# Kernel optimization log

Hardware: AMD Instinct MI355X
Metric: run time of the kernel (lower is better)

The kernel has to match this reference:

```python
import jax, jax.numpy as jnp
import numpy as np

N_NODES = 50000
N_EDGES = 800000
IN_C, HID_C, OUT_C = 128, 128, 64


def setup_inputs() -> dict:
    key = jax.random.key(0)
    ks = jax.random.split(key, 8)
    sc_in = 1.0 / np.sqrt(IN_C)
    sc_hid = 1.0 / np.sqrt(HID_C)
    return {
        "x": jax.random.normal(ks[0], (N_NODES, IN_C), dtype=jnp.float32),
        "edge_index": jax.random.randint(ks[1], (2, N_EDGES), 0, N_NODES, dtype=jnp.int64),
        "W1_l": jax.random.normal(ks[2], (IN_C, HID_C), dtype=jnp.float32) * sc_in,
        "b1": jnp.zeros((HID_C,), dtype=jnp.float32),
        "W1_r": jax.random.normal(ks[3], (IN_C, HID_C), dtype=jnp.float32) * sc_in,
        "W2_l": jax.random.normal(ks[4], (HID_C, OUT_C), dtype=jnp.float32) * sc_hid,
        "b2": jnp.zeros((OUT_C,), dtype=jnp.float32),
        "W2_r": jax.random.normal(ks[5], (HID_C, OUT_C), dtype=jnp.float32) * sc_hid,
    }


def _sage_conv(x, src, dst, W_l, b, W_r, num_nodes):
    # gather neighbor features along edges: messages flow src -> dst
    msg = x[src]                                             # [E, C]
    agg = jax.ops.segment_sum(msg, dst, num_segments=num_nodes)
    cnt = jax.ops.segment_sum(jnp.ones((src.shape[0],), x.dtype), dst,
                              num_segments=num_nodes)
    mean = agg / jnp.maximum(cnt, 1.0)[:, None]              # mean aggregation
    # PyG SAGEConv: lin_l(aggregated) + lin_r(root); bias on lin_l only
    return mean @ W_l + b + x @ W_r


def reference(x, edge_index, W1_l, b1, W1_r, W2_l, b2, W2_r):
    src, dst = edge_index[0], edge_index[1]
    n = x.shape[0]
    h = jax.nn.relu(_sage_conv(x, src, dst, W1_l, b1, W1_r, n))
    # dropout(p=0.2) is identity at inference (training=False)
    return _sage_conv(h, src, dst, W2_l, b2, W2_r, n)
```

## Files before the change

kernel.cpp:

```cpp
#include <hip/hip_runtime.h>

#define N_NODES 50000
#define N_EDGES 800000
#define IN_C 128
#define HID_C 128
#define OUT_C 64

#define NBUCK 500
#define NODES_PER_BUCK 100
#define BCAP 2560
#define BA_CHUNK 8192
#define BA_BLOCKS ((N_EDGES + BA_CHUNK - 1) / BA_CHUNK)

typedef __bf16 bf16x8 __attribute__((ext_vector_type(8)));
typedef __bf16 bf16x4 __attribute__((ext_vector_type(4)));
typedef float  f32x4  __attribute__((ext_vector_type(4)));


__global__ __launch_bounds__(256) void init_cursor_kernel(int* cursor) {
    int i = blockIdx.x * 256 + threadIdx.x;
    if (i < NBUCK) cursor[i] = i * BCAP;
}

__global__ __launch_bounds__(256) void bucketA_kernel(const int* __restrict__ src,
                                                      const int* __restrict__ dst,
                                                      int* __restrict__ cursor,
                                                      uint2* __restrict__ ebuf) {
    __shared__ int cnt[NBUCK];
    __shared__ int gbase[NBUCK];
    __shared__ int lcur[NBUCK];
    const int t = threadIdx.x;
    for (int i = t; i < NBUCK; i += 256) cnt[i] = 0;
    __syncthreads();
    const int e0 = blockIdx.x * BA_CHUNK;
    const int e1 = (e0 + BA_CHUNK < N_EDGES) ? e0 + BA_CHUNK : N_EDGES;
    for (int e = e0 + t; e < e1; e += 256)
        atomicAdd(&cnt[dst[e] / NODES_PER_BUCK], 1);
    __syncthreads();
    for (int i = t; i < NBUCK; i += 256) {
        gbase[i] = atomicAdd(&cursor[i], cnt[i]);
        lcur[i] = 0;
    }
    __syncthreads();
    for (int e = e0 + t; e < e1; e += 256) {
        int d = dst[e];
        int b = d / NODES_PER_BUCK;
        int idx = gbase[b] + atomicAdd(&lcur[b], 1);
        if (idx < (b + 1) * BCAP)
            ebuf[idx] = make_uint2((unsigned)src[e], (unsigned)d);
    }
}

__global__ __launch_bounds__(512) void scan500_kernel(const int* __restrict__ cursor,
                                                      int* __restrict__ bbase,
                                                      int* __restrict__ bsize) {
    __shared__ int sh[512];
    const int t = threadIdx.x;
    int v = 0;
    if (t < NBUCK) {
        v = cursor[t] - t * BCAP;
        if (v > BCAP) v = BCAP;
    }
    sh[t] = v;
    __syncthreads();
    for (int off = 1; off < 512; off <<= 1) {
        int u = (t >= off) ? sh[t - off] : 0;
        __syncthreads();
        sh[t] += u;
        __syncthreads();
    }
    if (t < NBUCK) { bbase[t] = sh[t] - v; bsize[t] = v; }
}

__global__ __launch_bounds__(256) void bucketB_kernel(const uint2* __restrict__ ebuf,
                                                      const int* __restrict__ bbase,
                                                      const int* __restrict__ bsize,
                                                      int* __restrict__ row_ptr,
                                                      int* __restrict__ srcs) {
    __shared__ int deg[NODES_PER_BUCK];
    __shared__ int ofs[NODES_PER_BUCK + 1];
    const int b = blockIdx.x, t = threadIdx.x;
    const int node0 = b * NODES_PER_BUCK;
    const int m = bsize[b];
    const int rbase = bbase[b];
    const uint2* eb = ebuf + (size_t)b * BCAP;
    for (int i = t; i < NODES_PER_BUCK; i += 256) deg[i] = 0;
    __syncthreads();
    for (int i = t; i < m; i += 256)
        atomicAdd(&deg[(int)eb[i].y - node0], 1);
    __syncthreads();
    if (t == 0) {
        int s = 0;
        for (int i = 0; i < NODES_PER_BUCK; ++i) { ofs[i] = s; s += deg[i]; }
        ofs[NODES_PER_BUCK] = s;
    }
    __syncthreads();
    for (int i = t; i < NODES_PER_BUCK; i += 256) row_ptr[node0 + i] = rbase + ofs[i];
    if (b == 0 && t == 0) row_ptr[N_NODES] = N_EDGES;
    for (int i = t; i < NODES_PER_BUCK; i += 256) deg[i] = ofs[i];
    __syncthreads();
    for (int i = t; i < m; i += 256) {
        uint2 p = eb[i];
        int d = (int)p.y - node0;
        int pos = atomicAdd(&deg[d], 1);
        srcs[rbase + pos] = (int)p.x;
    }
}


__global__ __launch_bounds__(256) void f32_to_bf16_kernel(const float* __restrict__ in,
                                                          __bf16* __restrict__ out, int n4) {
    int i = blockIdx.x * 256 + threadIdx.x;
    if (i >= n4) return;
    float4 v = ((const float4*)in)[i];
    bf16x4 o = { (__bf16)v.x, (__bf16)v.y, (__bf16)v.z, (__bf16)v.w };
    ((bf16x4*)out)[i] = o;
}

__global__ __launch_bounds__(256) void pack_w_kernel(const float* __restrict__ W1l,
                                                     const float* __restrict__ W1r,
                                                     const float* __restrict__ W2l,
                                                     const float* __restrict__ W2r,
                                                     __bf16* __restrict__ W1T,
                                                     __bf16* __restrict__ W2T) {
    int i = blockIdx.x * 256 + threadIdx.x;
    if (i < 128 * 256) {
        int n = i >> 8, kk = i & 255;
        float v = (kk < 128) ? W1l[kk * 128 + n] : W1r[(kk - 128) * 128 + n];
        W1T[i] = (__bf16)v;
    } else {
        int j = i - 128 * 256;
        if (j < 128 * 128) {
            int n = j >> 7, k = j & 127;
            float v = (n < 64) ? W2l[k * 64 + n] : W2r[k * 64 + (n - 64)];
            W2T[j] = (__bf16)v;
        }
    }
}

__global__ __launch_bounds__(256) void agg_x_kernel(const __bf16* __restrict__ xb,
                                                    const int* __restrict__ row_ptr,
                                                    const int* __restrict__ srcs,
                                                    __bf16* __restrict__ m1) {
    const int wid = threadIdx.x >> 6, lane = threadIdx.x & 63;
    const int n = blockIdx.x * 4 + wid;
    if (n >= N_NODES) return;
    const int beg = row_ptr[n], end = row_ptr[n + 1];
    const int grp = lane >> 4;
    const int c   = lane & 15;
    float acc[8] = {};
    for (int s = beg + grp; s < end; s += 4) {
        int u = srcs[s];
        bf16x8 v = *(const bf16x8*)(xb + (size_t)u * 128 + c * 8);
#pragma unroll
        for (int j = 0; j < 8; j++) acc[j] += (float)v[j];
    }
#pragma unroll
    for (int j = 0; j < 8; j++) {
        acc[j] += __shfl_xor(acc[j], 16, 64);
        acc[j] += __shfl_xor(acc[j], 32, 64);
    }
    float cnt = (float)(end - beg);
    if (cnt < 1.f) cnt = 1.f;
    if (grp == 0) {
        bf16x8 o;
#pragma unroll
        for (int j = 0; j < 8; j++) o[j] = (__bf16)(acc[j] / cnt);
        *(bf16x8*)(m1 + (size_t)n * 128 + c * 8) = o;
    }
}

#define LDK 72

__global__ __launch_bounds__(256) void gemm1_kernel(const __bf16* __restrict__ A0,
                                                    const __bf16* __restrict__ A1,
                                                    const __bf16* __restrict__ Bt,
                                                    const float* __restrict__ b1,
                                                    __bf16* __restrict__ h, int M) {
    __shared__ __bf16 As[128 * LDK];
    __shared__ __bf16 Bs[128 * LDK];
    const int tid = threadIdx.x;
    const int row0 = blockIdx.y * 128;
    const int wave = tid >> 6, lane = tid & 63;
    const int wm = (wave & 1) * 64, wn = (wave >> 1) * 64;
    const int lr = lane & 15, quad = lane >> 4;

    f32x4 acc[4][4] = {};

    for (int ks = 0; ks < 256; ks += 64) {
        const __bf16* Asrc = (ks < 128) ? A0 : A1;
        const int kofs = (ks < 128) ? ks : ks - 128;
        for (int i = tid; i < 128 * 8; i += 256) {
            int r = i >> 3, ch = i & 7;
            int gr = row0 + r;
            float4 v = {0.f, 0.f, 0.f, 0.f};
            if (gr < M) v = *(const float4*)(Asrc + (size_t)gr * 128 + kofs + ch * 8);
            *(float4*)(As + r * LDK + ch * 8) = v;
        }
        for (int i = tid; i < 128 * 8; i += 256) {
            int r = i >> 3, ch = i & 7;
            float4 v = *(const float4*)(Bt + (size_t)r * 256 + ks + ch * 8);
            *(float4*)(Bs + r * LDK + ch * 8) = v;
        }
        __syncthreads();
#pragma unroll
        for (int k0 = 0; k0 < 64; k0 += 32) {
            bf16x8 af[4], bfr[4];
#pragma unroll
            for (int mt = 0; mt < 4; mt++)
                af[mt] = *(const bf16x8*)(As + (wm + mt * 16 + lr) * LDK + k0 + quad * 8);
#pragma unroll
            for (int nt = 0; nt < 4; nt++)
                bfr[nt] = *(const bf16x8*)(Bs + (wn + nt * 16 + lr) * LDK + k0 + quad * 8);
#pragma unroll
            for (int mt = 0; mt < 4; mt++)
#pragma unroll
                for (int nt = 0; nt < 4; nt++)
                    acc[mt][nt] = __builtin_amdgcn_mfma_f32_16x16x32_bf16(af[mt], bfr[nt], acc[mt][nt], 0, 0, 0);
        }
        __syncthreads();
    }

#pragma unroll
    for (int mt = 0; mt < 4; mt++) {
#pragma unroll
        for (int r = 0; r < 4; r++) {
            int gr = row0 + wm + mt * 16 + quad * 4 + r;
            if (gr >= M) continue;
#pragma unroll
            for (int nt = 0; nt < 4; nt++) {
                int gc = wn + nt * 16 + lr;
                float v = acc[mt][nt][r] + b1[gc];
                v = v > 0.f ? v : 0.f;
                h[(size_t)gr * 128 + gc] = (__bf16)v;
            }
        }
    }
}

__global__ __launch_bounds__(256) void gemm2_kernel(const __bf16* __restrict__ A,
                                                    const __bf16* __restrict__ Bt,
                                                    __bf16* __restrict__ Y,
                                                    float* __restrict__ Z, int M) {
    __shared__ __bf16 As[128 * LDK];
    __shared__ __bf16 Bs[128 * LDK];
    const int tid = threadIdx.x;
    const int row0 = blockIdx.y * 128;
    const int wave = tid >> 6, lane = tid & 63;
    const int wm = (wave & 1) * 64, wn = (wave >> 1) * 64;
    const int lr = lane & 15, quad = lane >> 4;

    f32x4 acc[4][4] = {};

    for (int ks = 0; ks < 128; ks += 64) {
        for (int i = tid; i < 128 * 8; i += 256) {
            int r = i >> 3, ch = i & 7;
            int gr = row0 + r;
            float4 v = {0.f, 0.f, 0.f, 0.f};
            if (gr < M) v = *(const float4*)(A + (size_t)gr * 128 + ks + ch * 8);
            *(float4*)(As + r * LDK + ch * 8) = v;
        }
        for (int i = tid; i < 128 * 8; i += 256) {
            int r = i >> 3, ch = i & 7;
            float4 v = *(const float4*)(Bt + (size_t)r * 128 + ks + ch * 8);
            *(float4*)(Bs + r * LDK + ch * 8) = v;
        }
        __syncthreads();
#pragma unroll
        for (int k0 = 0; k0 < 64; k0 += 32) {
            bf16x8 af[4], bfr[4];
#pragma unroll
            for (int mt = 0; mt < 4; mt++)
                af[mt] = *(const bf16x8*)(As + (wm + mt * 16 + lr) * LDK + k0 + quad * 8);
#pragma unroll
            for (int nt = 0; nt < 4; nt++)
                bfr[nt] = *(const bf16x8*)(Bs + (wn + nt * 16 + lr) * LDK + k0 + quad * 8);
#pragma unroll
            for (int mt = 0; mt < 4; mt++)
#pragma unroll
                for (int nt = 0; nt < 4; nt++)
                    acc[mt][nt] = __builtin_amdgcn_mfma_f32_16x16x32_bf16(af[mt], bfr[nt], acc[mt][nt], 0, 0, 0);
        }
        __syncthreads();
    }

#pragma unroll
    for (int mt = 0; mt < 4; mt++) {
#pragma unroll
        for (int r = 0; r < 4; r++) {
            int gr = row0 + wm + mt * 16 + quad * 4 + r;
            if (gr >= M) continue;
#pragma unroll
            for (int nt = 0; nt < 4; nt++) {
                int gc = wn + nt * 16 + lr;
                float v = acc[mt][nt][r];
                if (gc < 64) Y[(size_t)gr * 64 + gc] = (__bf16)v;
                else         Z[(size_t)gr * 64 + (gc - 64)] = v;
            }
        }
    }
}

__global__ __launch_bounds__(256) void agg2_kernel(const __bf16* __restrict__ Y,
                                                   const float* __restrict__ Z,
                                                   const int* __restrict__ row_ptr,
                                                   const int* __restrict__ srcs,
                                                   const float* __restrict__ b2,
                                                   float* __restrict__ out) {
    const int wid = threadIdx.x >> 6, lane = threadIdx.x & 63;
    const int n = blockIdx.x * 4 + wid;
    if (n >= N_NODES) return;
    const int beg = row_ptr[n], end = row_ptr[n + 1];
    const int grp = lane >> 3;
    const int c   = lane & 7;
    float acc[8] = {};
    for (int s = beg + grp; s < end; s += 8) {
        int u = srcs[s];
        bf16x8 v = *(const bf16x8*)(Y + (size_t)u * 64 + c * 8);
#pragma unroll
        for (int j = 0; j < 8; j++) acc[j] += (float)v[j];
    }
#pragma unroll
    for (int j = 0; j < 8; j++) {
        acc[j] += __shfl_xor(acc[j], 8, 64);
        acc[j] += __shfl_xor(acc[j], 16, 64);
        acc[j] += __shfl_xor(acc[j], 32, 64);
    }
    float cnt = (float)(end - beg);
    if (cnt < 1.f) cnt = 1.f;
    if (grp == 0) {
#pragma unroll
        for (int j = 0; j < 8; j++) {
            int ch = c * 8 + j;
            out[(size_t)n * 64 + ch] = acc[j] / cnt + b2[ch] + Z[(size_t)n * 64 + ch];
        }
    }
}


extern "C" void kernel_launch(void* const* d_in, const int* in_sizes, int n_in,
                              void* d_out, int out_size, void* d_ws, size_t ws_size,
                              hipStream_t stream) {
    const float* x   = (const float*)d_in[0];
    const int*   ei  = (const int*)d_in[1];
    const float* W1l = (const float*)d_in[2];
    const float* b1  = (const float*)d_in[3];
    const float* W1r = (const float*)d_in[4];
    const float* W2l = (const float*)d_in[5];
    const float* b2  = (const float*)d_in[6];
    const float* W2r = (const float*)d_in[7];
    float* out = (float*)d_out;

    size_t need = 0;
    auto count = [&](size_t bytes) { need += (bytes + 255) & ~(size_t)255; };
    count((size_t)NBUCK * BCAP * 8);
    count((size_t)NBUCK * 4);
    count((size_t)NBUCK * 4);
    count((size_t)NBUCK * 4);
    count((size_t)(N_NODES + 1) * 4);
    count((size_t)N_EDGES * 4);
    count((size_t)N_NODES * 128 * 2);
    count((size_t)128 * 256 * 2);
    count((size_t)128 * 128 * 2);
    count((size_t)N_NODES * 128 * 2);
    count((size_t)N_NODES * 128 * 2);
    count((size_t)N_NODES * 64 * 2);
    count((size_t)N_NODES * 64 * 4);
    if (ws_size < need) return;

    char* ws = (char*)d_ws;
    size_t off = 0;
    auto alloc = [&](size_t bytes) -> void* {
        void* p = ws + off;
        off += (bytes + 255) & ~(size_t)255;
        return p;
    };
    uint2*  ebuf    = (uint2*)alloc((size_t)NBUCK * BCAP * 8);
    int*    cursor  = (int*)alloc((size_t)NBUCK * 4);
    int*    bbase   = (int*)alloc((size_t)NBUCK * 4);
    int*    bsize   = (int*)alloc((size_t)NBUCK * 4);
    int*    row_ptr = (int*)alloc((size_t)(N_NODES + 1) * 4);
    int*    srcs    = (int*)alloc((size_t)N_EDGES * 4);
    __bf16* xb      = (__bf16*)alloc((size_t)N_NODES * 128 * 2);
    __bf16* W1T     = (__bf16*)alloc((size_t)128 * 256 * 2);
    __bf16* W2T     = (__bf16*)alloc((size_t)128 * 128 * 2);
    __bf16* m1      = (__bf16*)alloc((size_t)N_NODES * 128 * 2);
    __bf16* h       = (__bf16*)alloc((size_t)N_NODES * 128 * 2);
    __bf16* Y       = (__bf16*)alloc((size_t)N_NODES * 64 * 2);
    float*  Z       = (float*)alloc((size_t)N_NODES * 64 * 4);

    const int* src = ei;
    const int* dst = ei + N_EDGES;

    init_cursor_kernel<<<(NBUCK + 255) / 256, 256, 0, stream>>>(cursor);
    bucketA_kernel<<<BA_BLOCKS, 256, 0, stream>>>(src, dst, cursor, ebuf);
    scan500_kernel<<<1, 512, 0, stream>>>(cursor, bbase, bsize);
    bucketB_kernel<<<NBUCK, 256, 0, stream>>>(ebuf, bbase, bsize, row_ptr, srcs);

    f32_to_bf16_kernel<<<(N_NODES * 128 / 4 + 255) / 256, 256, 0, stream>>>(x, xb, N_NODES * 128 / 4);
    pack_w_kernel<<<(128 * 256 + 128 * 128 + 255) / 256, 256, 0, stream>>>(W1l, W1r, W2l, W2r, W1T, W2T);

    agg_x_kernel<<<(N_NODES + 3) / 4, 256, 0, stream>>>(xb, row_ptr, srcs, m1);
    {
        dim3 grid(1, (N_NODES + 127) / 128);
        gemm1_kernel<<<grid, 256, 0, stream>>>(m1, xb, W1T, b1, h, N_NODES);
    }

    {
        dim3 grid(1, (N_NODES + 127) / 128);
        gemm2_kernel<<<grid, 256, 0, stream>>>(h, W2T, Y, Z, N_NODES);
    }
    agg2_kernel<<<(N_NODES + 3) / 4, 256, 0, stream>>>(Y, Z, row_ptr, srcs, b2, out);
}
```

Before: 224.4 us.

## Fuse GEMMs, merge prep kernels, inline bucket scan, unroll gathers

Merges the x→bf16 conversion, weight packing and cursor init into one prep kernel. Folds the 500-bucket scan into bucketB, where each block reduces its own prefix. Fuses gemm1 and gemm2 so the ReLU hidden tile stays in shared memory instead of round-tripping through HBM. Unrolls the edge gather loops in both aggregation kernels by two to raise memory-level parallelism. This removes several launches and about 25MB of intermediate traffic, at the cost of a larger LDS footprint and redundant prefix sums across bucketB blocks.

Result: faster. 203.7 us (-9.3%).

```diff
diff --git a/kernel.cpp b/kernel.cpp
--- a/kernel.cpp
+++ b/kernel.cpp
@@ -12,15 +12,47 @@
 #define BA_CHUNK 8192
 #define BA_BLOCKS ((N_EDGES + BA_CHUNK - 1) / BA_CHUNK)
 
+#define XB_BLOCKS 6250
+#define W1T_BLOCKS 128
+#define W2T_BLOCKS 64
+#define PREP_BLOCKS (XB_BLOCKS + W1T_BLOCKS + W2T_BLOCKS + 2)
+
 typedef __bf16 bf16x8 __attribute__((ext_vector_type(8)));
 typedef __bf16 bf16x4 __attribute__((ext_vector_type(4)));
 typedef float  f32x4  __attribute__((ext_vector_type(4)));
 
 
-__global__ __launch_bounds__(256) void init_cursor_kernel(int* cursor) {
-    int i = blockIdx.x * 256 + threadIdx.x;
-    if (i < NBUCK) cursor[i] = i * BCAP;
-}
+__global__ __launch_bounds__(256) void prep_kernel(const float* __restrict__ x,
+                                                   const float* __restrict__ W1l,
+                                                   const float* __restrict__ W1r,
+                                                   const float* __restrict__ W2l,
+                                                   const float* __restrict__ W2r,
+                                                   __bf16* __restrict__ xb,
+                                                   __bf16* __restrict__ W1T,
+                                                   __bf16* __restrict__ W2T,
+                                                   int* __restrict__ cursor) {
+    const int b = blockIdx.x, t = threadIdx.x;
+    if (b < XB_BLOCKS) {
+        int i = b * 256 + t;
+        float4 v = ((const float4*)x)[i];
+        bf16x4 o = { (__bf16)v.x, (__bf16)v.y, (__bf16)v.z, (__bf16)v.w };
+        ((bf16x4*)xb)[i] = o;
+    } else if (b < XB_BLOCKS + W1T_BLOCKS) {
+        int i = (b - XB_BLOCKS) * 256 + t;
+        int n = i >> 8, kk = i & 255;
+        float v = (kk < 128) ? W1l[kk * 128 + n] : W1r[(kk - 128) * 128 + n];
+        W1T[i] = (__bf16)v;
+    } else if (b < XB_BLOCKS + W1T_BLOCKS + W2T_BLOCKS) {
+        int i = (b - XB_BLOCKS - W1T_BLOCKS) * 256 + t;
+        int n = i >> 7, k = i & 127;
+        float v = (n < 64) ? W2l[k * 64 + n] : W2r[k * 64 + (n - 64)];
+        W2T[i] = (__bf16)v;
+    } else {
+        int i = (b - XB_BLOCKS - W1T_BLOCKS - W2T_BLOCKS) * 256 + t;
+        if (i < NBUCK) cursor[i] = i * BCAP;
+    }
+}
+
 
 __global__ __launch_bounds__(256) void bucketA_kernel(const int* __restrict__ src,
                                                       const int* __restrict__ dst,
@@ -51,39 +83,32 @@
     }
 }
 
-__global__ __launch_bounds__(512) void scan500_kernel(const int* __restrict__ cursor,
-                                                      int* __restrict__ bbase,
-                                                      int* __restrict__ bsize) {
-    __shared__ int sh[512];
-    const int t = threadIdx.x;
-    int v = 0;
-    if (t < NBUCK) {
-        v = cursor[t] - t * BCAP;
-        if (v > BCAP) v = BCAP;
-    }
-    sh[t] = v;
-    __syncthreads();
-    for (int off = 1; off < 512; off <<= 1) {
-        int u = (t >= off) ? sh[t - off] : 0;
-        __syncthreads();
-        sh[t] += u;
-        __syncthreads();
-    }
-    if (t < NBUCK) { bbase[t] = sh[t] - v; bsize[t] = v; }
-}
-
 __global__ __launch_bounds__(256) void bucketB_kernel(const uint2* __restrict__ ebuf,
-                                                      const int* __restrict__ bbase,
-                                                      const int* __restrict__ bsize,
+                                                      const int* __restrict__ cursor,
                                                       int* __restrict__ row_ptr,
                                                       int* __restrict__ srcs) {
+    __shared__ int psum[256];
     __shared__ int deg[NODES_PER_BUCK];
     __shared__ int ofs[NODES_PER_BUCK + 1];
     const int b = blockIdx.x, t = threadIdx.x;
+    int part = 0;
+    for (int i = t; i < b; i += 256) {
+        int c = cursor[i] - i * BCAP;
+        if (c > BCAP) c = BCAP;
+        part += c;
+    }
+    psum[t] = part;
+    __syncthreads();
+    for (int off = 128; off > 0; off >>= 1) {
+        if (t < off) psum[t] += psum[t + off];
+        __syncthreads();
+    }
+    const int rbase = psum[0];
+    int m = cursor[b] - b * BCAP;
+    if (m > BCAP) m = BCAP;
     const int node0 = b * NODES_PER_BUCK;
-    const int m = bsize[b];
-    const int rbase = bbase[b];
     const uint2* eb = ebuf + (size_t)b * BCAP;
+
     for (int i = t; i < NODES_PER_BUCK; i += 256) deg[i] = 0;
     __syncthreads();
     for (int i = t; i < m; i += 256)
@@ -104,37 +129,6 @@
         int d = (int)p.y - node0;
         int pos = atomicAdd(&deg[d], 1);
         srcs[rbase + pos] = (int)p.x;
-    }
-}
-
-
-__global__ __launch_bounds__(256) void f32_to_bf16_kernel(const float* __restrict__ in,
-                                                          __bf16* __restrict__ out, int n4) {
-    int i = blockIdx.x * 256 + threadIdx.x;
-    if (i >= n4) return;
-    float4 v = ((const float4*)in)[i];
-    bf16x4 o = { (__bf16)v.x, (__bf16)v.y, (__bf16)v.z, (__bf16)v.w };
-    ((bf16x4*)out)[i] = o;
-}
-
-__global__ __launch_bounds__(256) void pack_w_kernel(const float* __restrict__ W1l,
-                                                     const float* __restrict__ W1r,
-                                                     const float* __restrict__ W2l,
-                                                     const float* __restrict__ W2r,
-                                                     __bf16* __restrict__ W1T,
-                                                     __bf16* __restrict__ W2T) {
-    int i = blockIdx.x * 256 + threadIdx.x;
-    if (i < 128 * 256) {
-        int n = i >> 8, kk = i & 255;
-        float v = (kk < 128) ? W1l[kk * 128 + n] : W1r[(kk - 128) * 128 + n];
-        W1T[i] = (__bf16)v;
-    } else {
-        int j = i - 128 * 256;
-        if (j < 128 * 128) {
-            int n = j >> 7, k = j & 127;
-            float v = (n < 64) ? W2l[k * 64 + n] : W2r[k * 64 + (n - 64)];
-            W2T[j] = (__bf16)v;
-        }
     }
 }
 
@@ -149,7 +143,18 @@
     const int grp = lane >> 4;
     const int c   = lane & 15;
     float acc[8] = {};
-    for (int s = beg + grp; s < end; s += 4) {
+    int s = beg + grp;
+    for (; s + 4 < end; s += 8) {
+        int u0 = srcs[s];
+        int u1 = srcs[s + 4];
+        bf16x8 v0 = *(const bf16x8*)(xb + (size_t)u0 * 128 + c * 8);
+        bf16x8 v1 = *(const bf16x8*)(xb + (size_t)u1 * 128 + c * 8);
+#pragma unroll
+        for (int j = 0; j < 8; j++) acc[j] += (float)v0[j];
+#pragma unroll
+        for (int j = 0; j < 8; j++) acc[j] += (float)v1[j];
+    }
+    if (s < end) {
         int u = srcs[s];
         bf16x8 v = *(const bf16x8*)(xb + (size_t)u * 128 + c * 8);
 #pragma unroll
@@ -171,22 +176,24 @@
 }
 
 #define LDK 72
-
-__global__ __launch_bounds__(256) void gemm1_kernel(const __bf16* __restrict__ A0,
-                                                    const __bf16* __restrict__ A1,
-                                                    const __bf16* __restrict__ Bt,
-                                                    const float* __restrict__ b1,
-                                                    __bf16* __restrict__ h, int M) {
-    __shared__ __bf16 As[128 * LDK];
+#define LDH 136
+
+__global__ __launch_bounds__(256) void gemm12_kernel(const __bf16* __restrict__ A0,
+                                                     const __bf16* __restrict__ A1,
+                                                     const __bf16* __restrict__ W1T,
+                                                     const __bf16* __restrict__ W2T,
+                                                     const float* __restrict__ b1,
+                                                     __bf16* __restrict__ Y,
+                                                     float* __restrict__ Z, int M) {
+    __shared__ __bf16 As[128 * LDH];
     __shared__ __bf16 Bs[128 * LDK];
     const int tid = threadIdx.x;
-    const int row0 = blockIdx.y * 128;
+    const int row0 = blockIdx.x * 128;
     const int wave = tid >> 6, lane = tid & 63;
     const int wm = (wave & 1) * 64, wn = (wave >> 1) * 64;
     const int lr = lane & 15, quad = lane >> 4;
 
     f32x4 acc[4][4] = {};
-
     for (int ks = 0; ks < 256; ks += 64) {
         const __bf16* Asrc = (ks < 128) ? A0 : A1;
         const int kofs = (ks < 128) ? ks : ks - 128;
@@ -195,11 +202,11 @@
             int gr = row0 + r;
             float4 v = {0.f, 0.f, 0.f, 0.f};
             if (gr < M) v = *(const float4*)(Asrc + (size_t)gr * 128 + kofs + ch * 8);
-            *(float4*)(As + r * LDK + ch * 8) = v;
+            *(float4*)(As + r * LDH + ch * 8) = v;
         }
         for (int i = tid; i < 128 * 8; i += 256) {
             int r = i >> 3, ch = i & 7;
-            float4 v = *(const float4*)(Bt + (size_t)r * 256 + ks + ch * 8);
+            float4 v = *(const float4*)(W1T + (size_t)r * 256 + ks + ch * 8);
             *(float4*)(Bs + r * LDK + ch * 8) = v;
         }
         __syncthreads();
@@ -208,7 +215,7 @@
             bf16x8 af[4], bfr[4];
 #pragma unroll
             for (int mt = 0; mt < 4; mt++)
-                af[mt] = *(const bf16x8*)(As + (wm + mt * 16 + lr) * LDK + k0 + quad * 8);
+                af[mt] = *(const bf16x8*)(As + (wm + mt * 16 + lr) * LDH + k0 + quad * 8);
 #pragma unroll
             for (int nt = 0; nt < 4; nt++)
                 bfr[nt] = *(const bf16x8*)(Bs + (wn + nt * 16 + lr) * LDK + k0 + quad * 8);
@@ -217,6 +224,47 @@
 #pragma unroll
                 for (int nt = 0; nt < 4; nt++)
                     acc[mt][nt] = __builtin_amdgcn_mfma_f32_16x16x32_bf16(af[mt], bfr[nt], acc[mt][nt], 0, 0, 0);
+        }
+        __syncthreads();
+    }
+
+#pragma unroll
+    for (int mt = 0; mt < 4; mt++) {
+#pragma unroll
+        for (int r = 0; r < 4; r++) {
+            int row = wm + mt * 16 + quad * 4 + r;
+#pragma unroll
+            for (int nt = 0; nt < 4; nt++) {
+                int col = wn + nt * 16 + lr;
+                float v = acc[mt][nt][r] + b1[col];
+                v = v > 0.f ? v : 0.f;
+                As[row * LDH + col] = (__bf16)v;
+            }
+        }
+    }
+
+    f32x4 acc2[4][4] = {};
+    for (int kh = 0; kh < 128; kh += 64) {
+        for (int i = tid; i < 128 * 8; i += 256) {
+            int r = i >> 3, ch = i & 7;
+            float4 v = *(const float4*)(W2T + (size_t)r * 128 + kh + ch * 8);
+            *(float4*)(Bs + r * LDK + ch * 8) = v;
+        }
+        __syncthreads();
+#pragma unroll
+        for (int k0 = 0; k0 < 64; k0 += 32) {
+            bf16x8 af[4], bfr[4];
+#pragma unroll
+            for (int mt = 0; mt < 4; mt++)
+                af[mt] = *(const bf16x8*)(As + (wm + mt * 16 + lr) * LDH + kh + k0 + quad * 8);
+#pragma unroll
+            for (int nt = 0; nt < 4; nt++)
+                bfr[nt] = *(const bf16x8*)(Bs + (wn + nt * 16 + lr) * LDK + k0 + quad * 8);
+#pragma unroll
+            for (int mt = 0; mt < 4; mt++)
+#pragma unroll
+                for (int nt = 0; nt < 4; nt++)
+                    acc2[mt][nt] = __builtin_amdgcn_mfma_f32_16x16x32_bf16(af[mt], bfr[nt], acc2[mt][nt], 0, 0, 0);
         }
         __syncthreads();
     }
@@ -230,70 +278,7 @@
 #pragma unroll
             for (int nt = 0; nt < 4; nt++) {
                 int gc = wn + nt * 16 + lr;
-                float v = acc[mt][nt][r] + b1[gc];
-                v = v > 0.f ? v : 0.f;
-                h[(size_t)gr * 128 + gc] = (__bf16)v;
-            }
-        }
-    }
-}
-
-__global__ __launch_bounds__(256) void gemm2_kernel(const __bf16* __restrict__ A,
-                                                    const __bf16* __restrict__ Bt,
-                                                    __bf16* __restrict__ Y,
-                                                    float* __restrict__ Z, int M) {
-    __shared__ __bf16 As[128 * LDK];
-    __shared__ __bf16 Bs[128 * LDK];
-    const int tid = threadIdx.x;
-    const int row0 = blockIdx.y * 128;
-    const int wave = tid >> 6, lane = tid & 63;
-    const int wm = (wave & 1) * 64, wn = (wave >> 1) * 64;
-    const int lr = lane & 15, quad = lane >> 4;
-
-    f32x4 acc[4][4] = {};
-
-    for (int ks = 0; ks < 128; ks += 64) {
-        for (int i = tid; i < 128 * 8; i += 256) {
-            int r = i >> 3, ch = i & 7;
-            int gr = row0 + r;
-            float4 v = {0.f, 0.f, 0.f, 0.f};
-            if (gr < M) v = *(const float4*)(A + (size_t)gr * 128 + ks + ch * 8);
-            *(float4*)(As + r * LDK + ch * 8) = v;
-        }
-        for (int i = tid; i < 128 * 8; i += 256) {
-            int r = i >> 3, ch = i & 7;
-            float4 v = *(const float4*)(Bt + (size_t)r * 128 + ks + ch * 8);
-            *(float4*)(Bs + r * LDK + ch * 8) = v;
-        }
-        __syncthreads();
-#pragma unroll
-        for (int k0 = 0; k0 < 64; k0 += 32) {
-            bf16x8 af[4], bfr[4];
-#pragma unroll
-            for (int mt = 0; mt < 4; mt++)
-                af[mt] = *(const bf16x8*)(As + (wm + mt * 16 + lr) * LDK + k0 + quad * 8);
-#pragma unroll
-            for (int nt = 0; nt < 4; nt++)
-                bfr[nt] = *(const bf16x8*)(Bs + (wn + nt * 16 + lr) * LDK + k0 + quad * 8);
-#pragma unroll
-            for (int mt = 0; mt < 4; mt++)
-#pragma unroll
-                for (int nt = 0; nt < 4; nt++)
-                    acc[mt][nt] = __builtin_amdgcn_mfma_f32_16x16x32_bf16(af[mt], bfr[nt], acc[mt][nt], 0, 0, 0);
-        }
-        __syncthreads();
-    }
-
-#pragma unroll
-    for (int mt = 0; mt < 4; mt++) {
-#pragma unroll
-        for (int r = 0; r < 4; r++) {
-            int gr = row0 + wm + mt * 16 + quad * 4 + r;
-            if (gr >= M) continue;
-#pragma unroll
-            for (int nt = 0; nt < 4; nt++) {
-                int gc = wn + nt * 16 + lr;
-                float v = acc[mt][nt][r];
+                float v = acc2[mt][nt][r];
                 if (gc < 64) Y[(size_t)gr * 64 + gc] = (__bf16)v;
                 else         Z[(size_t)gr * 64 + (gc - 64)] = v;
             }
@@ -314,7 +299,18 @@
     const int grp = lane >> 3;
     const int c   = lane & 7;
     float acc[8] = {};
-    for (int s = beg + grp; s < end; s += 8) {
+    int s = beg + grp;
+    for (; s + 8 < end; s += 16) {
+        int u0 = srcs[s];
+        int u1 = srcs[s + 8];
+        bf16x8 v0 = *(const bf16x8*)(Y + (size_t)u0 * 64 + c * 8);
+        bf16x8 v1 = *(const bf16x8*)(Y + (size_t)u1 * 64 + c * 8);
+#pragma unroll
+        for (int j = 0; j < 8; j++) acc[j] += (float)v0[j];
+#pragma unroll
+        for (int j = 0; j < 8; j++) acc[j] += (float)v1[j];
+    }
+    if (s < end) {
         int u = srcs[s];
         bf16x8 v = *(const bf16x8*)(Y + (size_t)u * 64 + c * 8);
 #pragma unroll
@@ -355,14 +351,11 @@
     auto count = [&](size_t bytes) { need += (bytes + 255) & ~(size_t)255; };
     count((size_t)NBUCK * BCAP * 8);
     count((size_t)NBUCK * 4);
-    count((size_t)NBUCK * 4);
-    count((size_t)NBUCK * 4);
     count((size_t)(N_NODES + 1) * 4);
     count((size_t)N_EDGES * 4);
     count((size_t)N_NODES * 128 * 2);
     count((size_t)128 * 256 * 2);
     count((size_t)128 * 128 * 2);
-    count((size_t)N_NODES * 128 * 2);
     count((size_t)N_NODES * 128 * 2);
     count((size_t)N_NODES * 64 * 2);
     count((size_t)N_NODES * 64 * 4);
@@ -377,38 +370,22 @@
     };
     uint2*  ebuf    = (uint2*)alloc((size_t)NBUCK * BCAP * 8);
     int*    cursor  = (int*)alloc((size_t)NBUCK * 4);
-    int*    bbase   = (int*)alloc((size_t)NBUCK * 4);
-    int*    bsize   = (int*)alloc((size_t)NBUCK * 4);
     int*    row_ptr = (int*)alloc((size_t)(N_NODES + 1) * 4);
     int*    srcs    = (int*)alloc((size_t)N_EDGES * 4);
     __bf16* xb      = (__bf16*)alloc((size_t)N_NODES * 128 * 2);
     __bf16* W1T     = (__bf16*)alloc((size_t)128 * 256 * 2);
     __bf16* W2T     = (__bf16*)alloc((size_t)128 * 128 * 2);
     __bf16* m1      = (__bf16*)alloc((size_t)N_NODES * 128 * 2);
-    __bf16* h       = (__bf16*)alloc((size_t)N_NODES * 128 * 2);
     __bf16* Y       = (__bf16*)alloc((size_t)N_NODES * 64 * 2);
     float*  Z       = (float*)alloc((size_t)N_NODES * 64 * 4);
 
     const int* src = ei;
     const int* dst = ei + N_EDGES;
 
-    init_cursor_kernel<<<(NBUCK + 255) / 256, 256, 0, stream>>>(cursor);
+    prep_kernel<<<PREP_BLOCKS, 256, 0, stream>>>(x, W1l, W1r, W2l, W2r, xb, W1T, W2T, cursor);
     bucketA_kernel<<<BA_BLOCKS, 256, 0, stream>>>(src, dst, cursor, ebuf);
-    scan500_kernel<<<1, 512, 0, stream>>>(cursor, bbase, bsize);
-    bucketB_kernel<<<NBUCK, 256, 0, stream>>>(ebuf, bbase, bsize, row_ptr, srcs);
-
-    f32_to_bf16_kernel<<<(N_NODES * 128 / 4 + 255) / 256, 256, 0, stream>>>(x, xb, N_NODES * 128 / 4);
-    pack_w_kernel<<<(128 * 256 + 128 * 128 + 255) / 256, 256, 0, stream>>>(W1l, W1r, W2l, W2r, W1T, W2T);
-
+    bucketB_kernel<<<NBUCK, 256, 0, stream>>>(ebuf, cursor, row_ptr, srcs);
     agg_x_kernel<<<(N_NODES + 3) / 4, 256, 0, stream>>>(xb, row_ptr, srcs, m1);
-    {
-        dim3 grid(1, (N_NODES + 127) / 128);
-        gemm1_kernel<<<grid, 256, 0, stream>>>(m1, xb, W1T, b1, h, N_NODES);
-    }
-
-    {
-        dim3 grid(1, (N_NODES + 127) / 128);
-        gemm2_kernel<<<grid, 256, 0, stream>>>(h, W2T, Y, Z, N_NODES);
-    }
+    gemm12_kernel<<<(N_NODES + 127) / 128, 256, 0, stream>>>(m1, xb, W1T, W2T, b1, Y, Z, N_NODES);
     agg2_kernel<<<(N_NODES + 3) / 4, 256, 0, stream>>>(Y, Z, row_ptr, srcs, b2, out);
 }
```
